# Optimization experiments

Measured on AMD Instinct MI355X. Metric: run time of the kernel, lower is better.

Reference implementation:

```python
import jax, jax.numpy as jnp
import numpy as np
from jax import lax

NUM_CLASSES = 2
MAX_DET = 300
SCORE_THR = 0.001
IOU_THR = 0.7
EPS = 1e-7


def _probiou_pairwise(b):
    # b: [M,5] = (cx, cy, w, h, angle). Gaussian-based rotated-box IoU (ProbIoU).
    cx, cy, w, h, t = (b[:, i] for i in range(5))
    ct, st = jnp.cos(t), jnp.sin(t)
    w2, h2 = w * w / 12.0, h * h / 12.0
    a = w2 * ct * ct + h2 * st * st
    bb = w2 * st * st + h2 * ct * ct
    c = (w2 - h2) * ct * st
    x1, y1, a1, b1, c1 = cx[:, None], cy[:, None], a[:, None], bb[:, None], c[:, None]
    x2, y2, a2, b2, c2 = cx[None, :], cy[None, :], a[None, :], bb[None, :], c[None, :]
    denom = (a1 + a2) * (b1 + b2) - (c1 + c2) ** 2 + EPS
    t1 = 0.25 * ((a1 + a2) * (y1 - y2) ** 2 + (b1 + b2) * (x1 - x2) ** 2) / denom
    t2 = 0.5 * ((c1 + c2) * (x2 - x1) * (y1 - y2)) / denom
    det1 = jnp.maximum(a1 * b1 - c1 * c1, 0.0)
    det2 = jnp.maximum(a2 * b2 - c2 * c2, 0.0)
    t3 = 0.5 * jnp.log(denom / (4.0 * jnp.sqrt(det1 * det2) + EPS) + EPS)
    bd = jnp.clip(t1 + t2 + t3, EPS, 100.0)
    hd = jnp.sqrt(1.0 - jnp.exp(-bd) + EPS)
    return 1.0 - hd


def _nms_single(boxes5, scores):
    # boxes5: [N,5], scores: [N,C] -> class-aware greedy rotated NMS
    N, C = scores.shape
    M = N * C
    cand_boxes = jnp.broadcast_to(boxes5[:, None, :], (N, C, 5)).reshape(M, 5)
    cand_scores = scores.reshape(M)
    cand_labels = jnp.broadcast_to(jnp.arange(C, dtype=jnp.int32)[None, :], (N, C)).reshape(M)
    order = jnp.argsort(-cand_scores)
    b, s, l = cand_boxes[order], cand_scores[order], cand_labels[order]
    iou = _probiou_pairwise(b)                          # [M,M]
    same = l[:, None] == l[None, :]
    sup = (iou > IOU_THR) & same
    idx = jnp.arange(M)
    valid = s > SCORE_THR

    def body(i, keep):
        row = sup[i] & (idx > i) & keep[i]
        return keep & ~row

    keep = lax.fori_loop(0, M, body, valid)
    sel = jnp.where(keep, s, -1.0)
    top = jnp.argsort(-sel)[:MAX_DET]
    ok = sel[top] > 0.0
    out_boxes = jnp.where(ok[:, None], b[top], 0.0)     # [MAX_DET,5]
    out_scores = jnp.where(ok, s[top], 0.0)             # [MAX_DET]
    out_labels = jnp.where(ok, l[top], 0)               # [MAX_DET] int32
    n_valid = jnp.minimum(jnp.sum(keep), MAX_DET).astype(jnp.int32)
    return out_boxes, out_scores, out_labels, n_valid


def _forward(x, conv_w, conv_b, bbox_w, bbox_b, cls_w, cls_b, ang_w, ang_b):
    B = x.shape[0]
    f = lax.conv_general_dilated(x, conv_w, (1, 1), 'SAME',
                                 dimension_numbers=('NCHW', 'OIHW', 'NCHW'))
    f = jax.nn.relu(f + conv_b[None, :, None, None])
    f = lax.reduce_window(f, -jnp.inf, lax.max, (1, 1, 2, 2), (1, 1, 2, 2), 'VALID')
    Hp, Wp = f.shape[2], f.shape[3]
    hw = Hp * Wp
    # 1x1-conv heads (materialized like the original), then spatial mean
    boxes = (jnp.einsum('bchw,oc->bohw', f, bbox_w) + bbox_b[None, :, None, None]
             ).reshape(B, MAX_DET, 4, hw).mean(-1)
    logits = (jnp.einsum('bchw,oc->bohw', f, cls_w) + cls_b[None, :, None, None]
              ).reshape(B, MAX_DET, NUM_CLASSES, hw).mean(-1)
    scores = jax.nn.softmax(logits, axis=2)
    angles = (jnp.einsum('bchw,oc->bohw', f, ang_w) + ang_b[None, :, None, None]
              ).reshape(B, MAX_DET, 1, hw).mean(-1)
    boxes5 = jnp.concatenate([boxes, angles], axis=-1)  # [B,300,5]
    return jax.vmap(_nms_single)(boxes5, scores)


def setup_inputs() -> dict:
    key = jax.random.key(0)
    ks = jax.random.split(key, 10)
    B, H, W = 4, 256, 256
    s = 0.1
    return {
        'x': jax.random.normal(ks[0], (B, 3, H, W), jnp.float32),
        'conv_w': jax.random.normal(ks[1], (16, 3, 3, 3), jnp.float32) * s,
        'conv_b': jax.random.normal(ks[2], (16,), jnp.float32) * s,
        'bbox_w': jax.random.normal(ks[3], (4 * MAX_DET, 16), jnp.float32) * s,
        'bbox_b': jax.random.normal(ks[4], (4 * MAX_DET,), jnp.float32) * s,
        'cls_w': jax.random.normal(ks[5], (NUM_CLASSES * MAX_DET, 16), jnp.float32) * s,
        'cls_b': jax.random.normal(ks[6], (NUM_CLASSES * MAX_DET,), jnp.float32) * s,
        'ang_w': jax.random.normal(ks[7], (MAX_DET, 16), jnp.float32) * s,
        'ang_b': jax.random.normal(ks[8], (MAX_DET,), jnp.float32) * s,
    }


def reference(x, conv_w, conv_b, bbox_w, bbox_b, cls_w, cls_b, ang_w, ang_b):
    return _forward(x, conv_w, conv_b, bbox_w, bbox_b, cls_w, cls_b, ang_w, ang_b)
```

## Files before the change

### kernel.cpp

```cpp
#include <hip/hip_runtime.h>
#include <hip/hip_bf16.h>

#define MAX_DET 300
#define NCAND 600
#define NPAD 640
#define SCORE_THR 1e-3f
#define IOU_THR 0.7f
#define EPSF 1e-7f

typedef float float4u __attribute__((ext_vector_type(4), aligned(4)));


static __device__ inline unsigned long long readlane64(unsigned long long v, int l) {
  unsigned int lo = (unsigned int)v;
  unsigned int hi = (unsigned int)(v >> 32);
  unsigned int slo = (unsigned int)__builtin_amdgcn_readlane((int)lo, l);
  unsigned int shi = (unsigned int)__builtin_amdgcn_readlane((int)hi, l);
  return ((unsigned long long)shi << 32) | (unsigned long long)slo;
}

__global__ __launch_bounds__(256) void k_conv_pool(
    const float* __restrict__ x, const float* __restrict__ cw,
    const float* __restrict__ cb, float* __restrict__ partial) {
  const int blk = blockIdx.x;
  const int chunk = blk & 7;
  const int oc = (blk >> 3) & 15;
  const int b = blk >> 7;
  const int tid = threadIdx.x;

  float w[27];
#pragma unroll
  for (int i = 0; i < 27; ++i) w[i] = cw[oc * 27 + i];
  const float bias = cb[oc];
  const float* xb = x + b * 3 * 65536;

  const int strip = chunk * 256 + tid;
  const int py = strip >> 4;
  const int x0 = (strip & 15) * 8;

  float cc0[8], cc1[8], cc2[8], cc3[8];
#pragma unroll
  for (int i = 0; i < 8; ++i) { cc0[i] = 0.f; cc1[i] = 0.f; cc2[i] = 0.f; cc3[i] = 0.f; }

#pragma unroll
  for (int ic = 0; ic < 3; ++ic) {
    const float* xc = xb + ic * 65536;
    const float* wc = w + ic * 9;
#pragma unroll
    for (int r = 0; r < 4; ++r) {
      const int y = 2 * py - 1 + r;
      if (y < 0 || y > 255) continue;
      const float* xr = xc + y * 256;
      float buf[20];
#pragma unroll
      for (int k = 0; k < 5; ++k) {
        const int c0 = 2 * x0 - 1 + 4 * k;
        if (c0 >= 0 && c0 + 3 <= 255) {
          const float4u v = *reinterpret_cast<const float4u*>(xr + c0);
          buf[4 * k + 0] = v.x; buf[4 * k + 1] = v.y;
          buf[4 * k + 2] = v.z; buf[4 * k + 3] = v.w;
        } else {
#pragma unroll
          for (int j = 0; j < 4; ++j) {
            const int c = c0 + j;
            buf[4 * k + j] = (c >= 0 && c <= 255) ? xr[c] : 0.f;
          }
        }
      }
#pragma unroll
      for (int i = 0; i < 8; ++i) {
        const float b0 = buf[2 * i], b1 = buf[2 * i + 1],
                    b2 = buf[2 * i + 2], b3 = buf[2 * i + 3];
        if (r <= 2) {
          const float w0 = wc[r * 3], w1 = wc[r * 3 + 1], w2 = wc[r * 3 + 2];
          cc0[i] += b0 * w0 + b1 * w1 + b2 * w2;
          cc1[i] += b1 * w0 + b2 * w1 + b3 * w2;
        }
        if (r >= 1) {
          const float w0 = wc[(r - 1) * 3], w1 = wc[(r - 1) * 3 + 1],
                      w2 = wc[(r - 1) * 3 + 2];
          cc2[i] += b0 * w0 + b1 * w1 + b2 * w2;
          cc3[i] += b1 * w0 + b2 * w1 + b3 * w2;
        }
      }
    }
  }

  float acc = 0.f;
#pragma unroll
  for (int i = 0; i < 8; ++i) {
    const float m = fmaxf(fmaxf(cc0[i], cc1[i]), fmaxf(cc2[i], cc3[i]));
    acc += fmaxf(m + bias, 0.f);
  }

  __shared__ float red[256];
  red[tid] = acc;
  __syncthreads();
  for (int s = 128; s > 0; s >>= 1) {
    if (tid < s) red[tid] += red[tid + s];
    __syncthreads();
  }
  if (tid == 0) partial[blk] = red[0];
}

__global__ __launch_bounds__(1024) void k_prep(
    const float* __restrict__ partial,
    const float* __restrict__ bw, const float* __restrict__ bb,
    const float* __restrict__ cwm, const float* __restrict__ cbb,
    const float* __restrict__ aw, const float* __restrict__ ab,
    float* __restrict__ boxes5, float* __restrict__ sparams,
    int* __restrict__ order_g) {
  const int b = blockIdx.x;
  const int tid = threadIdx.x;
  const int wid = tid >> 6, lane = tid & 63;

  __shared__ float fm[16];
  __shared__ float sc[NPAD];
  __shared__ float sbox[MAX_DET * 5];
  __shared__ int order[NCAND];

  if (tid < 16) {
    float s = 0.f;
    for (int k = 0; k < 8; ++k) s += partial[(b * 16 + tid) * 8 + k];
    fm[tid] = s * (1.0f / 16384.0f);
  }
  for (int m = NCAND + tid; m < NPAD; m += 1024) sc[m] = -1e30f;
  __syncthreads();

  float f[16];
#pragma unroll
  for (int k = 0; k < 16; ++k) f[k] = fm[k];

  for (int o = tid; o < 4 * MAX_DET; o += 1024) {
    const float4u* wp = reinterpret_cast<const float4u*>(bw + o * 16);
    const float4u v0 = wp[0], v1 = wp[1], v2 = wp[2], v3 = wp[3];
    float wrow[16] = {v0.x, v0.y, v0.z, v0.w, v1.x, v1.y, v1.z, v1.w,
                      v2.x, v2.y, v2.z, v2.w, v3.x, v3.y, v3.z, v3.w};
    float acc = bb[o];
#pragma unroll
    for (int k = 0; k < 16; ++k) acc += wrow[k] * f[k];
    const int d = o >> 2, j = o & 3;
    sbox[d * 5 + j] = acc;
    boxes5[(b * MAX_DET + d) * 5 + j] = acc;
  }
  if (tid < MAX_DET) {
    const int o = tid;
    const float4u* wp = reinterpret_cast<const float4u*>(aw + o * 16);
    const float4u v0 = wp[0], v1 = wp[1], v2 = wp[2], v3 = wp[3];
    float wrow[16] = {v0.x, v0.y, v0.z, v0.w, v1.x, v1.y, v1.z, v1.w,
                      v2.x, v2.y, v2.z, v2.w, v3.x, v3.y, v3.z, v3.w};
    float acc = ab[o];
#pragma unroll
    for (int k = 0; k < 16; ++k) acc += wrow[k] * f[k];
    sbox[o * 5 + 4] = acc;
    boxes5[(b * MAX_DET + o) * 5 + 4] = acc;
  }
  if (tid >= 512 && tid < 512 + MAX_DET) {
    const int p = tid - 512;
    const float4u* wp0 = reinterpret_cast<const float4u*>(cwm + (2 * p) * 16);
    const float4u* wp1 = reinterpret_cast<const float4u*>(cwm + (2 * p + 1) * 16);
    const float4u u0 = wp0[0], u1 = wp0[1], u2 = wp0[2], u3 = wp0[3];
    const float4u t0 = wp1[0], t1 = wp1[1], t2 = wp1[2], t3 = wp1[3];
    float w0r[16] = {u0.x, u0.y, u0.z, u0.w, u1.x, u1.y, u1.z, u1.w,
                     u2.x, u2.y, u2.z, u2.w, u3.x, u3.y, u3.z, u3.w};
    float w1r[16] = {t0.x, t0.y, t0.z, t0.w, t1.x, t1.y, t1.z, t1.w,
                     t2.x, t2.y, t2.z, t2.w, t3.x, t3.y, t3.z, t3.w};
    float a0 = cbb[2 * p], a1 = cbb[2 * p + 1];
#pragma unroll
    for (int k = 0; k < 16; ++k) {
      a0 += w0r[k] * f[k];
      a1 += w1r[k] * f[k];
    }
    const float mx = fmaxf(a0, a1);
    const float e0 = expf(a0 - mx), e1 = expf(a1 - mx);
    const float inv = 1.f / (e0 + e1);
    sc[p * 2 + 0] = e0 * inv;
    sc[p * 2 + 1] = e1 * inv;
  }
  __syncthreads();

  float sreg[10];
#pragma unroll
  for (int k = 0; k < 10; ++k) sreg[k] = sc[k * 64 + lane];

  for (int t = 0; t < 38; ++t) {
    const int i = t * 16 + wid;
    if (i < NCAND) {
      const float si = sc[i];
      int r = 0;
#pragma unroll
      for (int k = 0; k < 10; ++k) {
        const int j = k * 64 + lane;
        const bool c = (sreg[k] > si) || (sreg[k] == si && j < i);
        r += (int)__popcll(__ballot(c));
      }
      if (lane == 0) order[r] = i;
    }
  }
  __syncthreads();

  float* P = sparams + b * 7 * NPAD;
  if (tid < NCAND) {
    const int r = tid;
    const int i = order[r];
    order_g[b * NPAD + r] = i;
    const float* bp = sbox + (i >> 1) * 5;
    const float cx = bp[0], cy = bp[1], w = bp[2], h = bp[3], t = bp[4];
    const float ct = cosf(t), st = sinf(t);
    const float w2 = w * w * (1.f / 12.f), h2 = h * h * (1.f / 12.f);
    const float a = w2 * ct * ct + h2 * st * st;
    const float bb2 = w2 * st * st + h2 * ct * ct;
    const float c = (w2 - h2) * ct * st;
    P[0 * NPAD + r] = cx;
    P[1 * NPAD + r] = cy;
    P[2 * NPAD + r] = a;
    P[3 * NPAD + r] = bb2;
    P[4 * NPAD + r] = c;
    P[5 * NPAD + r] = fmaxf(a * bb2 - c * c, 0.f);
    P[6 * NPAD + r] = sc[i];
  }
}

__global__ __launch_bounds__(256) void k_mask(
    const float* __restrict__ sparams, const int* __restrict__ order_g,
    unsigned long long* __restrict__ mask) {
  const int wid = threadIdx.x >> 6, lane = threadIdx.x & 63;
  const int g = blockIdx.x * 4 + wid;
  const int b = g / NCAND, i = g % NCAND;

  const float* P = sparams + b * 7 * NPAD;
  const int* og = order_g + b * NPAD;
  const float x1 = P[i], y1 = P[NPAD + i], a1 = P[2 * NPAD + i],
              b1 = P[3 * NPAD + i], c1 = P[4 * NPAD + i], d1 = P[5 * NPAD + i];
  const int li = og[i] & 1;

#pragma unroll
  for (int w = 0; w < 10; ++w) {
    const int j = w * 64 + lane;
    const int jc = j < NCAND ? j : NCAND - 1;
    const float x2 = P[jc], y2 = P[NPAD + jc], a2 = P[2 * NPAD + jc],
                b2 = P[3 * NPAD + jc], c2 = P[4 * NPAD + jc],
                d2 = P[5 * NPAD + jc];
    const float as = a1 + a2, bs = b1 + b2, cs = c1 + c2;
    const float dxx = x2 - x1, dyy = y1 - y2;
    const float denom = as * bs - cs * cs + EPSF;
    const float rden = 1.f / denom;
    const float t1v = 0.25f * (as * dyy * dyy + bs * dxx * dxx) * rden;
    const float t2v = 0.5f * (cs * dxx * dyy) * rden;
    const float t3v = 0.5f * logf(denom / (4.f * sqrtf(d1 * d2) + EPSF) + EPSF);
    float bd = t1v + t2v + t3v;
    bd = fminf(fmaxf(bd, EPSF), 100.f);
    const float hd = sqrtf(1.f - expf(-bd) + EPSF);
    const bool cond = (j > i) && (j < NCAND) && ((og[jc] & 1) == li) &&
                      ((1.f - hd) > IOU_THR);
    const unsigned long long mw = __ballot(cond);
    if (lane == 0) mask[(b * NCAND + i) * 10 + w] = mw;
  }
}

__global__ __launch_bounds__(1024) void k_scan(
    const float* __restrict__ boxes5, const float* __restrict__ sparams,
    const int* __restrict__ order_g, const unsigned long long* __restrict__ mask,
    float* __restrict__ out) {
  const int b = blockIdx.x;
  const int tid = threadIdx.x;
  const int wid = tid >> 6, lane = tid & 63;

  __shared__ unsigned long long m[NCAND * 10];
  __shared__ float ssc[NCAND];
  __shared__ unsigned long long keepw[10];
  __shared__ unsigned long long validbm[10];
  __shared__ unsigned long long nzbm[10];

  const unsigned long long* mg = mask + b * NCAND * 10;
  for (int k = tid; k < NCAND * 10; k += 1024) m[k] = mg[k];
  const float* P = sparams + b * 7 * NPAD;
  if (tid < NCAND) ssc[tid] = P[6 * NPAD + tid];
  __syncthreads();

  if (wid < 10) {
    const int r = wid * 64 + lane;
    bool valid = false;
    unsigned long long nzr = 0ULL;
    if (r < NCAND) {
      valid = ssc[r] > SCORE_THR;
      for (int k = 0; k < 10; ++k) nzr |= m[r * 10 + k];
    }
    const unsigned long long vb = __ballot(valid);
    const unsigned long long nb = __ballot(nzr != 0ULL);
    if (lane == 0) { validbm[wid] = vb; nzbm[wid] = nb; }
  }
  __syncthreads();

  if (tid < 64) {
    unsigned long long keep = (lane < 10) ? validbm[lane] : 0ULL;
    const unsigned long long nzv = (lane < 10) ? nzbm[lane] : 0ULL;
#pragma unroll
    for (int w = 0; w < 10; ++w) {
      unsigned long long nzs = readlane64(nzv, w);
      unsigned long long ks = readlane64(keep, w);
      while (nzs) {
        const int bit = __builtin_ctzll(nzs);
        nzs &= nzs - 1ULL;
        if ((ks >> bit) & 1ULL) {
          const int i = w * 64 + bit;
          unsigned long long row = 0ULL;
          if (lane < 10) row = m[i * 10 + lane];
          keep &= ~row;
          ks &= ~readlane64(row, w);
        }
      }
    }
    if (lane < 10) keepw[lane] = keep;
  }
  __syncthreads();

  for (int k = tid; k < MAX_DET * 5; k += 1024) out[b * MAX_DET * 5 + k] = 0.f;
  if (tid < MAX_DET) {
    out[6000 + b * MAX_DET + tid] = 0.f;
    out[7200 + b * MAX_DET + tid] = 0.f;
  }
  __syncthreads();

  const int* og = order_g + b * NPAD;
  if (tid < NCAND) {
    const int r = tid;
    const int w = r >> 6, bitp = r & 63;
    if ((keepw[w] >> bitp) & 1ULL) {
      int pos = 0;
      for (int ww = 0; ww < w; ++ww) pos += __popcll(keepw[ww]);
      pos += __popcll(keepw[w] & ((1ULL << bitp) - 1ULL));
      if (pos < MAX_DET) {
        const int i = og[r];
        const float* bp = boxes5 + (b * MAX_DET + (i >> 1)) * 5;
        float* ob = out + (b * MAX_DET + pos) * 5;
        ob[0] = bp[0]; ob[1] = bp[1]; ob[2] = bp[2]; ob[3] = bp[3]; ob[4] = bp[4];
        out[6000 + b * MAX_DET + pos] = ssc[r];
        out[7200 + b * MAX_DET + pos] = (float)(i & 1);
      }
    }
  }
  if (tid == 0) {
    int total = 0;
    for (int ww = 0; ww < 10; ++ww) total += __popcll(keepw[ww]);
    if (total > MAX_DET) total = MAX_DET;
    out[8400 + b] = (float)total;
  }
}

extern "C" void kernel_launch(void* const* d_in, const int* in_sizes, int n_in,
                              void* d_out, int out_size, void* d_ws, size_t ws_size,
                              hipStream_t stream) {
  const float* x      = (const float*)d_in[0];
  const float* conv_w = (const float*)d_in[1];
  const float* conv_b = (const float*)d_in[2];
  const float* bbox_w = (const float*)d_in[3];
  const float* bbox_b = (const float*)d_in[4];
  const float* cls_w  = (const float*)d_in[5];
  const float* cls_b  = (const float*)d_in[6];
  const float* ang_w  = (const float*)d_in[7];
  const float* ang_b  = (const float*)d_in[8];
  float* out = (float*)d_out;
  float* ws = (float*)d_ws;

  float* partial = ws;
  float* boxes5  = ws + 1024;
  float* sparams = ws + 8720;
  int*   order_g = (int*)(ws + 26640);
  unsigned long long* mask = (unsigned long long*)(ws + 29200);

  k_conv_pool<<<512, 256, 0, stream>>>(x, conv_w, conv_b, partial);
  k_prep<<<4, 1024, 0, stream>>>(partial, bbox_w, bbox_b, cls_w, cls_b,
                                 ang_w, ang_b, boxes5, sparams, order_g);
  k_mask<<<600, 256, 0, stream>>>(sparams, order_g, mask);
  k_scan<<<4, 1024, 0, stream>>>(boxes5, sparams, order_g, mask, out);
}
```

Before: 59.57 us.

## Load input window once per pixel and loop over all output channels

The conv+pool kernel now gives each thread one pooled pixel, loads its 3x4x4 input window once, and computes all 16 output channels from it. Before, each block handled a single channel, so the input was re-read 16 times. The per-channel sums use wavefront shuffles instead of a shared-memory tree, and the grid halves to 256 blocks, with 64 partials per (batch, channel) reduced in two stages in k_prep. This cuts global input traffic and reduction syncs, at the cost of fewer blocks, scalar weight loads inside a non-unrolled oc loop, and a slightly longer reduction in k_prep.

```diff
diff --git a/kernel.cpp b/kernel.cpp
--- a/kernel.cpp
+++ b/kernel.cpp
@@ -23,84 +23,72 @@
     const float* __restrict__ x, const float* __restrict__ cw,
     const float* __restrict__ cb, float* __restrict__ partial) {
   const int blk = blockIdx.x;
-  const int chunk = blk & 7;
-  const int oc = (blk >> 3) & 15;
-  const int b = blk >> 7;
+  const int grp = blk & 63;
+  const int b = blk >> 6;
   const int tid = threadIdx.x;
-
-  float w[27];
-#pragma unroll
-  for (int i = 0; i < 27; ++i) w[i] = cw[oc * 27 + i];
-  const float bias = cb[oc];
+  const int lane = tid & 63, wid = tid >> 6;
+
+  const int p = grp * 256 + tid;
+  const int py = p >> 7, px = p & 127;
   const float* xb = x + b * 3 * 65536;
 
-  const int strip = chunk * 256 + tid;
-  const int py = strip >> 4;
-  const int x0 = (strip & 15) * 8;
-
-  float cc0[8], cc1[8], cc2[8], cc3[8];
-#pragma unroll
-  for (int i = 0; i < 8; ++i) { cc0[i] = 0.f; cc1[i] = 0.f; cc2[i] = 0.f; cc3[i] = 0.f; }
-
+  float win[3][4][4];
 #pragma unroll
   for (int ic = 0; ic < 3; ++ic) {
     const float* xc = xb + ic * 65536;
-    const float* wc = w + ic * 9;
 #pragma unroll
     for (int r = 0; r < 4; ++r) {
       const int y = 2 * py - 1 + r;
-      if (y < 0 || y > 255) continue;
-      const float* xr = xc + y * 256;
-      float buf[20];
-#pragma unroll
-      for (int k = 0; k < 5; ++k) {
-        const int c0 = 2 * x0 - 1 + 4 * k;
-        if (c0 >= 0 && c0 + 3 <= 255) {
-          const float4u v = *reinterpret_cast<const float4u*>(xr + c0);
-          buf[4 * k + 0] = v.x; buf[4 * k + 1] = v.y;
-          buf[4 * k + 2] = v.z; buf[4 * k + 3] = v.w;
-        } else {
-#pragma unroll
-          for (int j = 0; j < 4; ++j) {
-            const int c = c0 + j;
-            buf[4 * k + j] = (c >= 0 && c <= 255) ? xr[c] : 0.f;
-          }
+      const int c0 = 2 * px - 1;
+      if (y >= 0 && y <= 255 && c0 >= 0 && c0 + 3 <= 255) {
+        const float4u v = *reinterpret_cast<const float4u*>(xc + y * 256 + c0);
+        win[ic][r][0] = v.x; win[ic][r][1] = v.y;
+        win[ic][r][2] = v.z; win[ic][r][3] = v.w;
+      } else {
+#pragma unroll
+        for (int j = 0; j < 4; ++j) {
+          const int c = c0 + j;
+          win[ic][r][j] =
+              (y >= 0 && y <= 255 && c >= 0 && c <= 255) ? xc[y * 256 + c] : 0.f;
         }
       }
-#pragma unroll
-      for (int i = 0; i < 8; ++i) {
-        const float b0 = buf[2 * i], b1 = buf[2 * i + 1],
-                    b2 = buf[2 * i + 2], b3 = buf[2 * i + 3];
+    }
+  }
+
+  __shared__ float red[4 * 16];
+  for (int oc = 0; oc < 16; ++oc) {
+    float c0 = 0.f, c1 = 0.f, c2 = 0.f, c3 = 0.f;
+#pragma unroll
+    for (int ic = 0; ic < 3; ++ic) {
+      const float* wc = cw + oc * 27 + ic * 9;
+#pragma unroll
+      for (int r = 0; r < 4; ++r) {
+        const float b0 = win[ic][r][0], b1 = win[ic][r][1],
+                    b2 = win[ic][r][2], b3 = win[ic][r][3];
         if (r <= 2) {
           const float w0 = wc[r * 3], w1 = wc[r * 3 + 1], w2 = wc[r * 3 + 2];
-          cc0[i] += b0 * w0 + b1 * w1 + b2 * w2;
-          cc1[i] += b1 * w0 + b2 * w1 + b3 * w2;
+          c0 += b0 * w0 + b1 * w1 + b2 * w2;
+          c1 += b1 * w0 + b2 * w1 + b3 * w2;
         }
         if (r >= 1) {
           const float w0 = wc[(r - 1) * 3], w1 = wc[(r - 1) * 3 + 1],
                       w2 = wc[(r - 1) * 3 + 2];
-          cc2[i] += b0 * w0 + b1 * w1 + b2 * w2;
-          cc3[i] += b1 * w0 + b2 * w1 + b3 * w2;
+          c2 += b0 * w0 + b1 * w1 + b2 * w2;
+          c3 += b1 * w0 + b2 * w1 + b3 * w2;
         }
       }
     }
-  }
-
-  float acc = 0.f;
-#pragma unroll
-  for (int i = 0; i < 8; ++i) {
-    const float m = fmaxf(fmaxf(cc0[i], cc1[i]), fmaxf(cc2[i], cc3[i]));
-    acc += fmaxf(m + bias, 0.f);
-  }
-
-  __shared__ float red[256];
-  red[tid] = acc;
-  __syncthreads();
-  for (int s = 128; s > 0; s >>= 1) {
-    if (tid < s) red[tid] += red[tid + s];
-    __syncthreads();
-  }
-  if (tid == 0) partial[blk] = red[0];
+    const float m = fmaxf(fmaxf(c0, c1), fmaxf(c2, c3));
+    float v = fmaxf(m + cb[oc], 0.f);
+#pragma unroll
+    for (int s = 1; s < 64; s <<= 1) v += __shfl_xor(v, s, 64);
+    if (lane == 0) red[wid * 16 + oc] = v;
+  }
+  __syncthreads();
+  if (tid < 16) {
+    const float s = red[tid] + red[16 + tid] + red[32 + tid] + red[48 + tid];
+    partial[(b * 16 + tid) * 64 + grp] = s;
+  }
 }
 
 __global__ __launch_bounds__(1024) void k_prep(
@@ -115,16 +103,26 @@
   const int wid = tid >> 6, lane = tid & 63;
 
   __shared__ float fm[16];
+  __shared__ float red2[256];
   __shared__ float sc[NPAD];
   __shared__ float sbox[MAX_DET * 5];
   __shared__ int order[NCAND];
 
+  if (tid < 256) {
+    const int oc = tid >> 4, k0 = (tid & 15) * 4;
+    float s = 0.f;
+#pragma unroll
+    for (int j = 0; j < 4; ++j) s += partial[(b * 16 + oc) * 64 + k0 + j];
+    red2[tid] = s;
+  }
+  for (int m = NCAND + tid; m < NPAD; m += 1024) sc[m] = -1e30f;
+  __syncthreads();
   if (tid < 16) {
     float s = 0.f;
-    for (int k = 0; k < 8; ++k) s += partial[(b * 16 + tid) * 8 + k];
+#pragma unroll
+    for (int k = 0; k < 16; ++k) s += red2[tid * 16 + k];
     fm[tid] = s * (1.0f / 16384.0f);
   }
-  for (int m = NCAND + tid; m < NPAD; m += 1024) sc[m] = -1e30f;
   __syncthreads();
 
   float f[16];
@@ -369,7 +367,7 @@
   int*   order_g = (int*)(ws + 26640);
   unsigned long long* mask = (unsigned long long*)(ws + 29200);
 
-  k_conv_pool<<<512, 256, 0, stream>>>(x, conv_w, conv_b, partial);
+  k_conv_pool<<<256, 256, 0, stream>>>(x, conv_w, conv_b, partial);
   k_prep<<<4, 1024, 0, stream>>>(partial, bbox_w, bbox_b, cls_w, cls_b,
                                  ang_w, ang_b, boxes5, sparams, order_g);
   k_mask<<<600, 256, 0, stream>>>(sparams, order_g, mask);
```

After: 63.50 us. 6.6% more time.
